# Kernel tuning notes

Measured on AMD Instinct MI355X. Metric: run time of the kernel, lower is better.

The kernel has to match this reference:

```python
import jax, jax.numpy as jnp
import numpy as np

B = 65536        # Monte-Carlo batch of samples
N_ORB = 64       # hilbert.n_orbitals (sites per spin sector)
NF_UP = 16       # hilbert.n_fermions_per_spin[0]
NF_DN = 16       # hilbert.n_fermions_per_spin[1]
NF = NF_UP + NF_DN  # hilbert.n_fermions


def setup_inputs() -> dict:
    key = jax.random.key(0)
    k1, k2, k3 = jax.random.split(key, 3)

    def occupancy(k, nf):
        # exactly nf ones among N_ORB orbitals per sample
        u = jax.random.uniform(k, (B, N_ORB))
        idx = jnp.argsort(-u, axis=1)[:, :nf]
        o = jnp.zeros((B, N_ORB), jnp.int32)
        return o.at[jnp.arange(B)[:, None], idx].set(1)

    n = jnp.concatenate([occupancy(k1, NF_UP), occupancy(k2, NF_DN)], axis=1)  # [B, 2*N_ORB]
    # backflow model: single dense layer n -> F (he-uniform-like scale)
    W = jax.random.normal(k3, (2 * N_ORB, N_ORB * NF), jnp.float32) / np.float32(np.sqrt(2 * N_ORB))
    return {"n": n, "W": W}


def _log_det(A):
    # complex log-determinant of batched real matrices
    sign, logabs = jnp.linalg.slogdet(A)
    return logabs.astype(jnp.complex64) + jnp.log(sign.astype(jnp.complex64))


def reference(n, W):
    F = n.astype(W.dtype) @ W                   # [B, N_ORB*NF] backflow orbitals
    M = F.reshape(-1, N_ORB, NF)                # [B, N_ORB, NF]
    n_u = n[:, :N_ORB]
    n_d = n[:, N_ORB:]
    # occupied-orbital indices in ascending order (== nonzero(size=nf)),
    # using a stable sort on the "unoccupied" flag
    R_u = jnp.argsort(n_u <= 0, axis=1)[:, :NF_UP]   # [B, NF_UP]
    R_d = jnp.argsort(n_d <= 0, axis=1)[:, :NF_DN]   # [B, NF_DN]
    A_u = jnp.take_along_axis(M[:, :, :NF_UP], R_u[:, :, None], axis=1)  # [B, NF_UP, NF_UP]
    A_d = jnp.take_along_axis(M[:, :, NF_UP:], R_d[:, :, None], axis=1)  # [B, NF_DN, NF_DN]
    return _log_det(A_u) + _log_det(A_d)        # [B] complex64
```

## Files before the change

### kernel.cpp

```cpp
#include <hip/hip_runtime.h>
#include <math.h>

#define NB 32
#define SLAB_F 4096
#define NSLAB 64
#define UNI_F 10240


typedef float f32x2 __attribute__((ext_vector_type(2)));
typedef float f32x4 __attribute__((ext_vector_type(4)));

#define GLD_LDS16(gp, lp) __builtin_amdgcn_global_load_lds( \
    (const __attribute__((address_space(1))) void*)(gp),    \
    (__attribute__((address_space(3))) void*)(lp), 16, 0, 0)

#define PKADD(acc, half) asm("v_pk_add_f32 %0, %0, %1" : "+v"(acc) : "v"(half))

__global__ __launch_bounds__(512, 4) void backflow_kernel(
    const int* __restrict__ nocc,
    const float* __restrict__ W,
    float* __restrict__ out,
    int B)
{
    __shared__ __align__(16) float uni[UNI_F];
    __shared__ int lists[NB][33];

    const int tid = threadIdx.x;

    {
        const int bib1 = tid >> 4;
        const int l16  = tid & 15;
        int batch1 = blockIdx.x * NB + bib1;
        if (batch1 >= B) batch1 = B - 1;
        const int4* np = reinterpret_cast<const int4*>(nocc + (size_t)batch1 * 128 + l16 * 8);
        int4 v0 = np[0];
        int4 v1 = np[1];
        unsigned nib = 0;
        nib |= (v0.x != 0) ? 1u   : 0u;
        nib |= (v0.y != 0) ? 2u   : 0u;
        nib |= (v0.z != 0) ? 4u   : 0u;
        nib |= (v0.w != 0) ? 8u   : 0u;
        nib |= (v1.x != 0) ? 16u  : 0u;
        nib |= (v1.y != 0) ? 32u  : 0u;
        nib |= (v1.z != 0) ? 64u  : 0u;
        nib |= (v1.w != 0) ? 128u : 0u;
        const int cnt = __popc(nib);
        int incl = cnt;
        const int seg = l16 & 7;
        #pragma unroll
        for (int d = 1; d < 8; d <<= 1) {
            int t = __shfl_up(incl, d, 8);
            if (seg >= d) incl += t;
        }
        int pos = ((l16 >> 3) << 4) + (incl - cnt);
        const int k0 = l16 * 8;
        #pragma unroll
        for (int b = 0; b < 8; b++) {
            if (nib & (1u << b)) lists[bib1][pos++] = k0 + b;
        }
        if (l16 == 0) lists[bib1][32] = 1 << 30;
    }
    __syncthreads();

    const int lane = tid & 63;
    const int wv   = __builtin_amdgcn_readfirstlane(tid >> 6);
    const int wb0  = wv << 2;

    const int rowidx = lane >> 1;
    const int h      = lane & 1;
    const int m2     = rowidx >> 4;
    const int rot    = rowidx & 1;

    const int col_l = (wv << 8) + (lane << 2);
    const char* gp0 = (const char*)(W + col_l);
    const char* gp1 = (const char*)(W + 2048 + col_l);
    char* const lb_base = (char*)uni + (wv << 10);

    GLD_LDS16(gp0, lb_base);
    GLD_LDS16(gp1, lb_base + 8192);
    gp0 += 16384; gp1 += 16384;

    int offs[4][2];
    int ptr4[4], nk4[4];
    #pragma unroll
    for (int b = 0; b < 4; b++) {
        const int ro = lists[wb0 + b][rowidx] - (m2 << 6);
        offs[b][0] = (ro << 7) + (m2 << 6) + (h << 5) + ((0 ^ rot) << 4);
        offs[b][1] = (ro << 7) + (m2 << 6) + (h << 5) + ((1 ^ rot) << 4);
        ptr4[b] = 0;
        nk4[b] = lists[wb0 + b][0];
    }

    f32x2 acc[4][4] = {};

    __syncthreads();

    #pragma unroll 1
    for (int s = 0; s < NSLAB; s++) {
        if (s < NSLAB - 1) {
            char* lb = (char*)uni + (((s + 1) & 1) << 14) + (wv << 10);
            GLD_LDS16(gp0, lb);
            GLD_LDS16(gp1, lb + 8192);
            gp0 += 16384; gp1 += 16384;
        }
        const char* cpB = (const char*)uni + ((s & 1) << 14);
        const int kend = (s << 1) + 2;
        #pragma unroll
        for (int b = 0; b < 4; b++) {
            while (nk4[b] < kend) {
                const char* kp = cpB + ((nk4[b] & 1) << 13);
                f32x4 v0 = *reinterpret_cast<const f32x4*>(kp + offs[b][0]);
                f32x4 v1 = *reinterpret_cast<const f32x4*>(kp + offs[b][1]);
                PKADD(acc[b][0], v0.lo); PKADD(acc[b][1], v0.hi);
                PKADD(acc[b][2], v1.lo); PKADD(acc[b][3], v1.hi);
                ptr4[b]++;
                nk4[b] = lists[wb0 + b][ptr4[b]];
            }
        }
        __syncthreads();
    }

    const int g   = lane >> 3;
    const int s8  = lane & 7;
    const int m   = g & 1;
    const int bwl = g >> 1;
    int batch = blockIdx.x * NB + wb0 + bwl;
    const bool valid = (batch < B);
    if (!valid) batch = B - 1;

    float* const sw = uni + wv * 1280;
    float* const wr = sw + rowidx * 20 + (h << 3);
    float a0[16], a1[16];

    {
        f32x4 t;
        t.lo = acc[0][0]; t.hi = acc[0][1];
        *reinterpret_cast<f32x4*>(wr + ((0 ^ rot) << 2)) = t;
        t.lo = acc[0][2]; t.hi = acc[0][3];
        *reinterpret_cast<f32x4*>(wr + ((1 ^ rot) << 2)) = t;
        t.lo = acc[1][0]; t.hi = acc[1][1];
        *reinterpret_cast<f32x4*>(wr + 640 + ((0 ^ rot) << 2)) = t;
        t.lo = acc[1][2]; t.hi = acc[1][3];
        *reinterpret_cast<f32x4*>(wr + 640 + ((1 ^ rot) << 2)) = t;
    }
    asm volatile("s_waitcnt lgkmcnt(0)" ::: "memory");
    __builtin_amdgcn_sched_barrier(0);
    if (lane < 32) {
        const float* r0 = sw + bwl * 640 + (m * 16 + s8) * 20;
        const float* r1 = r0 + 160;
        #pragma unroll
        for (int qq = 0; qq < 4; qq++) {
            f32x4 u0 = *reinterpret_cast<const f32x4*>(r0 + qq * 4);
            f32x4 u1 = *reinterpret_cast<const f32x4*>(r1 + qq * 4);
            a0[qq*4+0] = u0.x; a0[qq*4+1] = u0.y; a0[qq*4+2] = u0.z; a0[qq*4+3] = u0.w;
            a1[qq*4+0] = u1.x; a1[qq*4+1] = u1.y; a1[qq*4+2] = u1.z; a1[qq*4+3] = u1.w;
        }
    }
    asm volatile("s_waitcnt lgkmcnt(0)" ::: "memory");
    __builtin_amdgcn_sched_barrier(0);
    {
        f32x4 t;
        t.lo = acc[2][0]; t.hi = acc[2][1];
        *reinterpret_cast<f32x4*>(wr + ((0 ^ rot) << 2)) = t;
        t.lo = acc[2][2]; t.hi = acc[2][3];
        *reinterpret_cast<f32x4*>(wr + ((1 ^ rot) << 2)) = t;
        t.lo = acc[3][0]; t.hi = acc[3][1];
        *reinterpret_cast<f32x4*>(wr + 640 + ((0 ^ rot) << 2)) = t;
        t.lo = acc[3][2]; t.hi = acc[3][3];
        *reinterpret_cast<f32x4*>(wr + 640 + ((1 ^ rot) << 2)) = t;
    }
    asm volatile("s_waitcnt lgkmcnt(0)" ::: "memory");
    __builtin_amdgcn_sched_barrier(0);
    if (lane >= 32) {
        const float* r0 = sw + (bwl - 2) * 640 + (m * 16 + s8) * 20;
        const float* r1 = r0 + 160;
        #pragma unroll
        for (int qq = 0; qq < 4; qq++) {
            f32x4 u0 = *reinterpret_cast<const f32x4*>(r0 + qq * 4);
            f32x4 u1 = *reinterpret_cast<const f32x4*>(r1 + qq * 4);
            a0[qq*4+0] = u0.x; a0[qq*4+1] = u0.y; a0[qq*4+2] = u0.z; a0[qq*4+3] = u0.w;
            a1[qq*4+0] = u1.x; a1[qq*4+1] = u1.y; a1[qq*4+2] = u1.z; a1[qq*4+3] = u1.w;
        }
    }

    unsigned active = 0xffffu;
    int inv = 0;
    float myd0 = 1.f, myd1 = 1.f;

    #pragma unroll
    for (int k = 0; k < 16; k++) {
        const unsigned act0 = (active >> s8) & 1u;
        const unsigned act1 = (active >> (s8 + 8)) & 1u;
        float av = act0 ? fabsf(a0[k]) : -1.f;
        int idx = s8;
        {
            float av1 = act1 ? fabsf(a1[k]) : -1.f;
            if (av1 > av) { av = av1; idx = s8 + 8; }
        }
        #pragma unroll
        for (int d = 1; d < 8; d <<= 1) {
            float ov = __shfl_xor(av, d, 8);
            int   oi = __shfl_xor(idx, d, 8);
            if (ov > av || (ov == av && oi < idx)) { av = ov; idx = oi; }
        }
        const int p = idx;
        const int plane = p & 7;
        const bool phi = (p & 8) != 0;
        float psel = phi ? a1[k] : a0[k];
        const float pk = __shfl(psel, plane, 8);
        const float rcp = 1.0f / pk;

        if (s8 == p)     myd0 = pk;
        if (s8 + 8 == p) myd1 = pk;
        inv += __popc(active & ((1u << p) - 1u));
        active &= ~(1u << p);

        const float f0 = (act0 && s8 != p)       ? a0[k] * rcp : 0.f;
        const float f1 = (act1 && (s8 + 8) != p) ? a1[k] * rcp : 0.f;

        #pragma unroll
        for (int j = k + 1; j < 16; j++) {
            float sel = phi ? a1[j] : a0[j];
            float pv = __shfl(sel, plane, 8);
            a0[j] = fmaf(-f0, pv, a0[j]);
            a1[j] = fmaf(-f1, pv, a1[j]);
        }
    }

    float ld = logf(fabsf(myd0)) + logf(fabsf(myd1));
    int ng = ((myd0 < 0.f) ? 1 : 0) + ((myd1 < 0.f) ? 1 : 0);
    #pragma unroll
    for (int d = 1; d < 8; d <<= 1) {
        ld += __shfl_xor(ld, d, 8);
        ng += __shfl_xor(ng, d, 8);
    }
    const int neg = (ng + inv) & 1;

    const float ld_o  = __shfl_xor(ld, 8, 16);
    const int   neg_o = __shfl_xor(neg, 8, 16);

    if ((lane & 15) == 0 && valid) {
        out[batch]     = ld + ld_o;
        out[B + batch] = 3.14159265358979323846f * (float)(neg + neg_o);
    }
}

extern "C" void kernel_launch(void* const* d_in, const int* in_sizes, int n_in,
                              void* d_out, int out_size, void* d_ws, size_t ws_size,
                              hipStream_t stream) {
    const int* nocc = (const int*)d_in[0];
    const float* W  = (const float*)d_in[1];
    float* out = (float*)d_out;
    const int B = in_sizes[0] / 128;
    const int blocks = (B + NB - 1) / NB;
    backflow_kernel<<<blocks, 512, 0, stream>>>(nocc, W, out, B);
}
```

Baseline: 261.2 us.

## Stream W one row per step through a 4-deep LDS ring with occupancy bitmasks

Replaces the 2-row double-buffered slab loop with a 4-stage ring that loads one 8KB row of W per step, issuing three loads ahead and waiting with explicit vmcnt counts plus a raw s_barrier. The per-batch sorted occupied-index list walk, with its LDS list reads and while loops, is replaced by wave ballots over the occupancy vector that give 64-bit masks, so each step becomes a uniform bit test. This aims to hide global-load latency more deeply and drop the LDS lookups from the inner loop. In exchange it doubles the number of loop iterations and barriers and re-reads the occupancy array from global memory.

```diff
diff --git a/kernel.cpp b/kernel.cpp
--- a/kernel.cpp
+++ b/kernel.cpp
@@ -2,8 +2,7 @@
 #include <math.h>
 
 #define NB 32
-#define SLAB_F 4096
-#define NSLAB 64
+#define NSLAB 128
 #define UNI_F 10240
 
 
@@ -58,7 +57,6 @@
         for (int b = 0; b < 8; b++) {
             if (nib & (1u << b)) lists[bib1][pos++] = k0 + b;
         }
-        if (l16 == 0) lists[bib1][32] = 1 << 30;
     }
     __syncthreads();
 
@@ -71,54 +69,62 @@
     const int m2     = rowidx >> 4;
     const int rot    = rowidx & 1;
 
-    const int col_l = (wv << 8) + (lane << 2);
-    const char* gp0 = (const char*)(W + col_l);
-    const char* gp1 = (const char*)(W + 2048 + col_l);
-    char* const lb_base = (char*)uni + (wv << 10);
-
-    GLD_LDS16(gp0, lb_base);
-    GLD_LDS16(gp1, lb_base + 8192);
-    gp0 += 16384; gp1 += 16384;
+    unsigned long long mlo[4], mhi[4];
+    #pragma unroll
+    for (int b = 0; b < 4; b++) {
+        int gb = blockIdx.x * NB + wb0 + b;
+        if (gb >= B) gb = B - 1;
+        const int* npb = nocc + (size_t)gb * 128;
+        const int vlo = npb[lane];
+        const int vhi = npb[64 + lane];
+        mlo[b] = __ballot(vlo != 0);
+        mhi[b] = __ballot(vhi != 0);
+    }
 
     int offs[4][2];
-    int ptr4[4], nk4[4];
     #pragma unroll
     for (int b = 0; b < 4; b++) {
         const int ro = lists[wb0 + b][rowidx] - (m2 << 6);
         offs[b][0] = (ro << 7) + (m2 << 6) + (h << 5) + ((0 ^ rot) << 4);
         offs[b][1] = (ro << 7) + (m2 << 6) + (h << 5) + ((1 ^ rot) << 4);
-        ptr4[b] = 0;
-        nk4[b] = lists[wb0 + b][0];
     }
 
     f32x2 acc[4][4] = {};
 
-    __syncthreads();
+    const int col_l = (wv << 8) + (lane << 2);
+    const char* gp = (const char*)(W + col_l);
+    asm volatile("s_waitcnt vmcnt(0)" ::: "memory");
+    __builtin_amdgcn_sched_barrier(0);
+    #pragma unroll
+    for (int i = 0; i < 3; i++) {
+        GLD_LDS16(gp, (char*)uni + i * 8192 + (wv << 10));
+        gp += 8192;
+    }
 
     #pragma unroll 1
     for (int s = 0; s < NSLAB; s++) {
-        if (s < NSLAB - 1) {
-            char* lb = (char*)uni + (((s + 1) & 1) << 14) + (wv << 10);
-            GLD_LDS16(gp0, lb);
-            GLD_LDS16(gp1, lb + 8192);
-            gp0 += 16384; gp1 += 16384;
-        }
-        const char* cpB = (const char*)uni + ((s & 1) << 14);
-        const int kend = (s << 1) + 2;
+        if (s < NSLAB - 2)      asm volatile("s_waitcnt vmcnt(2) lgkmcnt(0)" ::: "memory");
+        else if (s == NSLAB - 2) asm volatile("s_waitcnt vmcnt(1) lgkmcnt(0)" ::: "memory");
+        else                     asm volatile("s_waitcnt vmcnt(0) lgkmcnt(0)" ::: "memory");
+        __builtin_amdgcn_s_barrier();
+        __builtin_amdgcn_sched_barrier(0);
+        if (s < NSLAB - 3) {
+            GLD_LDS16(gp, (char*)uni + ((s + 3) & 3) * 8192 + (wv << 10));
+            gp += 8192;
+        }
+        const char* kp = (const char*)uni + ((s & 3) << 13);
         #pragma unroll
         for (int b = 0; b < 4; b++) {
-            while (nk4[b] < kend) {
-                const char* kp = cpB + ((nk4[b] & 1) << 13);
-                f32x4 v0 = *reinterpret_cast<const f32x4*>(kp + offs[b][0]);
-                f32x4 v1 = *reinterpret_cast<const f32x4*>(kp + offs[b][1]);
+            const bool occ = (((s < 64 ? (mlo[b] >> s) : (mhi[b] >> (s - 64))) & 1ull) != 0);
+            if (occ) {
+                const f32x4 v0 = *reinterpret_cast<const f32x4*>(kp + offs[b][0]);
+                const f32x4 v1 = *reinterpret_cast<const f32x4*>(kp + offs[b][1]);
                 PKADD(acc[b][0], v0.lo); PKADD(acc[b][1], v0.hi);
                 PKADD(acc[b][2], v1.lo); PKADD(acc[b][3], v1.hi);
-                ptr4[b]++;
-                nk4[b] = lists[wb0 + b][ptr4[b]];
             }
         }
-        __syncthreads();
-    }
+    }
+    __syncthreads();
 
     const int g   = lane >> 3;
     const int s8  = lane & 7;
```

Measured after the change: 401.5 us. +53.7%, slower.
